# Performance work log

Measured on AMD Instinct MI355X. Metric: run time of the kernel, lower is better.

## Reference

```python
import jax, jax.numpy as jnp
import numpy as np
from jax import lax

NG = 2   # n_groups
NH = 4   # n_heads
LN_EPS = 1e-5

SOBEL_X = np.array([[-1., 0., 1.], [-2., 0., 2.], [-1., 0., 1.]], np.float32)
SOBEL_Y = np.array([[-1., -2., -1.], [0., 0., 0.], [1., 2., 1.]], np.float32)


def conv1x1(x, w, b=None):
    # x: (N, Ci, H, W), w: (Co, Ci)
    y = jnp.einsum('oi,bihw->bohw', w, x)
    if b is not None:
        y = y + b[None, :, None, None]
    return y


def dwconv3(x, w, b=None):
    # depthwise 3x3, stride 1, padding 1. w: (C, 1, 3, 3)
    y = lax.conv_general_dilated(x, w, (1, 1), ((1, 1), (1, 1)),
                                 feature_group_count=x.shape[1],
                                 dimension_numbers=('NCHW', 'OIHW', 'NCHW'))
    if b is not None:
        y = y + b[None, :, None, None]
    return y


def grid_sample_bilinear(img, grid):
    # img: (N, C, H, W); grid: (N, Hg, Wg, 2) with (x, y) in [-1, 1]
    # align_corners=True, zero padding (matches F.grid_sample defaults used here)
    N, C, H, W = img.shape
    gx = (grid[..., 0] + 1.0) * 0.5 * (W - 1)
    gy = (grid[..., 1] + 1.0) * 0.5 * (H - 1)
    x0 = jnp.floor(gx)
    y0 = jnp.floor(gy)
    wx1 = gx - x0
    wy1 = gy - y0

    def gather(yy, xx):
        valid = (yy >= 0) & (yy < H) & (xx >= 0) & (xx < W)
        yc = jnp.clip(yy, 0, H - 1).astype(jnp.int32)
        xc = jnp.clip(xx, 0, W - 1).astype(jnp.int32)
        vals = jax.vmap(lambda im, y_, x_: im[:, y_, x_])(img, yc, xc)  # (N,C,Hg,Wg)
        return vals * valid[:, None, :, :].astype(img.dtype)

    v00 = gather(y0, x0)
    v01 = gather(y0, x0 + 1)
    v10 = gather(y0 + 1, x0)
    v11 = gather(y0 + 1, x0 + 1)
    w00 = ((1 - wy1) * (1 - wx1))[:, None]
    w01 = ((1 - wy1) * wx1)[:, None]
    w10 = (wy1 * (1 - wx1))[:, None]
    w11 = (wy1 * wx1)[:, None]
    return v00 * w00 + v01 * w01 + v10 * w10 + v11 * w11


def setup_inputs() -> dict:
    key = jax.random.key(0)
    B, C, H, W = 4, 128, 48, 48
    Cg = C // NG
    ks = jax.random.split(key, 16)
    s = 0.02
    inp = {
        'x': jax.random.normal(ks[0], (B, C, H, W), jnp.float32),
        'qW': jax.random.normal(ks[1], (C, C), jnp.float32) * s,
        'qb': jnp.zeros((C,), jnp.float32),
        'kW': jax.random.normal(ks[2], (C, C), jnp.float32) * s,
        'kb': jnp.zeros((C,), jnp.float32),
        'vW': jax.random.normal(ks[3], (C, C), jnp.float32) * s,
        'vb': jnp.zeros((C,), jnp.float32),
        'oW': jax.random.normal(ks[4], (C, C), jnp.float32) * s,
        'ob': jnp.zeros((C,), jnp.float32),
        'off_dw_w': jax.random.normal(ks[5], (Cg, 1, 3, 3), jnp.float32) * 0.1,
        'off_dw_b': jnp.zeros((Cg,), jnp.float32),
        'ln_g': jnp.ones((Cg,), jnp.float32),
        'ln_b': jnp.zeros((Cg,), jnp.float32),
        'off_pw_w': jax.random.normal(ks[6], (2, Cg), jnp.float32) * s,
        'sob_w': jax.random.normal(ks[7], (1, Cg), jnp.float32) * 0.1,
        'sob_b': jnp.zeros((1,), jnp.float32),
        'rpe_w': jax.random.normal(ks[8], (C, 1, 3, 3), jnp.float32) * 0.1,
        'rpe_b': jnp.zeros((C,), jnp.float32),
    }
    return inp


def reference(x, qW, qb, kW, kb, vW, vb, oW, ob, off_dw_w, off_dw_b,
              ln_g, ln_b, off_pw_w, sob_w, sob_b, rpe_w, rpe_b):
    B, C, H, W = x.shape
    Cg = C // NG
    Dh = C // NH
    scale = Dh ** -0.5

    q = conv1x1(x, qW, qb)                                   # (B,C,H,W)
    q_off = q.reshape(B * NG, Cg, H, W)                      # (Bg,Cg,H,W)

    # offset branch: dwconv -> LayerNorm(channel) -> GELU -> 1x1 (no bias)
    t = dwconv3(q_off, off_dw_w, off_dw_b)
    tt = t.transpose(0, 2, 3, 1)                             # (Bg,H,W,Cg)
    mu = tt.mean(-1, keepdims=True)
    var = tt.var(-1, keepdims=True)
    tt = (tt - mu) / jnp.sqrt(var + LN_EPS) * ln_g + ln_b
    t = jax.nn.gelu(tt, approximate=False).transpose(0, 3, 1, 2)
    offset = conv1x1(t, off_pw_w)                            # (Bg,2,H,W)

    Hk, Wk = H, W
    n_sample = Hk * Wk
    off_range = jnp.array([1.0 / (Hk - 1.0), 1.0 / (Wk - 1.0)], x.dtype).reshape(1, 2, 1, 1)
    offset = jnp.tanh(offset) * off_range                    # offset_range_factor = 1
    offset = offset.transpose(0, 2, 3, 1)                    # (Bg,Hk,Wk,2)  (y,x)

    # reference points, normalized to [-1,1]
    ref_y = (jnp.linspace(0.5, Hk - 0.5, Hk, dtype=x.dtype) / (Hk - 1.0)) * 2.0 - 1.0
    ref_x = (jnp.linspace(0.5, Wk - 0.5, Wk, dtype=x.dtype) / (Wk - 1.0)) * 2.0 - 1.0
    ref = jnp.stack(jnp.meshgrid(ref_y, ref_x, indexing='ij'), axis=-1)  # (Hk,Wk,2)
    reference = jnp.broadcast_to(ref[None], (B * NG, Hk, Wk, 2))

    # Sobel gate on 1x1-projected q_off
    s = conv1x1(q_off, sob_w, sob_b)                         # (Bg,1,H,W)
    kx = jnp.asarray(SOBEL_X).reshape(1, 1, 3, 3)
    ky = jnp.asarray(SOBEL_Y).reshape(1, 1, 3, 3)
    gxm = dwconv3(s, kx)
    gym = dwconv3(s, ky)
    mag = jnp.sqrt(gxm ** 2 + gym ** 2)
    binary = (mag > 0.5).astype(x.dtype).transpose(0, 2, 3, 1)  # (Bg,H,W,1)

    pos = offset + reference * binary                        # (Bg,Hk,Wk,2) (y,x)

    xs = grid_sample_bilinear(x.reshape(B * NG, Cg, H, W), pos[..., ::-1])  # grid in (x,y)
    xs = xs.reshape(B, C, 1, n_sample)

    qf = q.reshape(B * NH, Dh, H * W)
    k = conv1x1(xs, kW, kb).reshape(B * NH, Dh, n_sample)
    v = conv1x1(xs, vW, vb).reshape(B * NH, Dh, n_sample)

    attn = jnp.einsum('bcm,bcn->bmn', qf, k) * scale         # (B*NH, HW, n_sample)
    lepe = dwconv3(q.reshape(B, C, H, W), rpe_w, rpe_b).reshape(B * NH, Dh, H * W)
    attn = jax.nn.softmax(attn, axis=2)                      # attn_drop: eval identity
    out = jnp.einsum('bmn,bcn->bcm', attn, v) + lepe
    out = out.reshape(B, C, H, W)
    y = conv1x1(out, oW, ob)                                 # proj_drop: eval identity
    return (y, pos, reference)
```

## Files before the change

### kernel.cpp

```cpp
#include <hip/hip_runtime.h>
#include <hip/hip_bf16.h>
#include <math.h>

#define B_   4
#define C_   128
#define H_   48
#define W_   48
#define HW_  2304
#define CG_  64
#define DH_  32
#define SCALE_ 0.17677669529663687f
#define QS_    (0.17677669529663687f * 1.4426950408889634f)
#define INVQ_  (1.0f / QS_)

#define Y_OFF   0
#define POS_OFF 1179648
#define REF_OFF 1216512

#define OFF_XTBF  0
#define OFF_QBF   589824
#define OFF_KBF   1179648
#define OFF_VBF   1769472
#define OFF_XST   2359296
#define OFF_WBF   2949120
#define OFF_PRS   2981888
#define OFF_PROH  4161536
#define OFF_AOUTT 6594560
#define OFF_SMAPD 7184384
#define OFF_WEFF  7221248

typedef __attribute__((ext_vector_type(8))) short short8;
typedef __attribute__((ext_vector_type(4))) float f32x4;
typedef __attribute__((ext_vector_type(4))) _Float16 f16x4;

__device__ inline unsigned short f2bf(float f) {
  unsigned u = __float_as_uint(f);
  u += 0x7fff + ((u >> 16) & 1);
  return (unsigned short)(u >> 16);
}
__device__ inline float bf2f(unsigned short s) {
  return __uint_as_float(((unsigned)s) << 16);
}

__device__ inline short8 pack8(const f32x4 a, const f32x4 b) {
  union { unsigned u[4]; short8 s; } r;
  asm("v_cvt_pk_bf16_f32 %0, %1, %2" : "=v"(r.u[0]) : "v"(a[0]), "v"(a[1]));
  asm("v_cvt_pk_bf16_f32 %0, %1, %2" : "=v"(r.u[1]) : "v"(a[2]), "v"(a[3]));
  asm("v_cvt_pk_bf16_f32 %0, %1, %2" : "=v"(r.u[2]) : "v"(b[0]), "v"(b[1]));
  asm("v_cvt_pk_bf16_f32 %0, %1, %2" : "=v"(r.u[3]) : "v"(b[2]), "v"(b[3]));
  return r.s;
}

__global__ __launch_bounds__(256) void k_pre(const float* __restrict__ x,
                                             const float* __restrict__ qW, const float* __restrict__ kW,
                                             const float* __restrict__ vW, const float* __restrict__ oW,
                                             const float* __restrict__ qb,
                                             const float* __restrict__ sob_w, const float* __restrict__ sob_b,
                                             unsigned short* __restrict__ xTbf,
                                             unsigned short* __restrict__ wbf,
                                             double* __restrict__ weff) {
  int bx = blockIdx.x;
  if (bx < 288) {
    __shared__ float tile[64][65];
    int p0 = (bx % 36) * 64, c0 = ((bx / 36) & 1) * 64, b = bx / 72;
    for (int idx = threadIdx.x; idx < 4096; idx += 256) {
      int cr = idx >> 6, pc = idx & 63;
      tile[cr][pc] = x[((size_t)(b * C_) + c0 + cr) * HW_ + p0 + pc];
    }
    __syncthreads();
    for (int idx = threadIdx.x; idx < 4096; idx += 256) {
      int pr = idx >> 6, cc = idx & 63;
      xTbf[((size_t)(b * HW_) + p0 + pr) * C_ + c0 + cc] = f2bf(tile[cc][pr]);
    }
  } else if (bx < 544) {
    int t = (bx - 288) * 256 + threadIdx.x;
    int which = t >> 14, i = t & 16383;
    const float* src = which == 0 ? qW : which == 1 ? kW : which == 2 ? vW : oW;
    wbf[t] = f2bf(src[i]);
  } else {
    int t = threadIdx.x;
    int g = t >> 7, i = t & 127;
    double acc = 0.0;
    for (int c = 0; c < 64; c++)
      acc += (double)sob_w[c] * (double)qW[(size_t)(g * 64 + c) * C_ + i];
    weff[t] = acc;
    if (t < 2) {
      double bb = (double)sob_b[0];
      for (int c = 0; c < 64; c++) bb += (double)sob_w[c] * (double)qb[t * 64 + c];
      weff[256 + t] = bb;
    }
  }
}

__global__ __launch_bounds__(256, 4) void k_qconv_smapd(const unsigned short* __restrict__ xTbf,
                                                        const unsigned short* __restrict__ wbf,
                                                        const float* __restrict__ qb,
                                                        const float* __restrict__ x,
                                                        const double* __restrict__ weff,
                                                        unsigned short* __restrict__ qbf,
                                                        double* __restrict__ smapd) {
  int bx = blockIdx.x;
  if (bx < 576) {
    int t = threadIdx.x, w = t >> 6, l = t & 63, lg = l >> 4, lo = l & 15;
    int m0 = (bx % 144) * 16, b = bx / 144, o0 = w * 32;
    const unsigned short* xrow = xTbf + ((size_t)(b * HW_) + m0 + lo) * C_ + lg * 8;
    f32x4 acc[2] = {{0.f,0.f,0.f,0.f},{0.f,0.f,0.f,0.f}};
#pragma unroll
    for (int kb = 0; kb < 4; kb++) {
      short8 xf = *(const short8*)(xrow + kb * 32);
#pragma unroll
      for (int os = 0; os < 2; os++) {
        short8 wf = *(const short8*)(wbf + (size_t)(o0 + os * 16 + lo) * C_ + kb * 32 + lg * 8);
        acc[os] = __builtin_amdgcn_mfma_f32_16x16x32_bf16(xf, wf, acc[os], 0, 0, 0);
      }
    }
#pragma unroll
    for (int os = 0; os < 2; os++) {
      int o = o0 + os * 16 + lo;
      float bi = qb[o];
#pragma unroll
      for (int r = 0; r < 4; r++) {
        int m = m0 + lg * 4 + r;
        qbf[((size_t)(b * HW_) + m) * C_ + o] = f2bf((acc[os][r] + bi) * QS_);
      }
    }
  } else {
    int bb = bx - 576;
    int p = (bb % 9) * 256 + threadIdx.x;
    int bg = bb / 9;
    int b = bg >> 1, g = bg & 1;
    const float* xb = x + (size_t)b * C_ * HW_ + p;
    const double* wv = weff + g * 128;
    double acc = weff[256 + g];
#pragma unroll 8
    for (int i = 0; i < 128; i++) acc += wv[i] * (double)xb[(size_t)i * HW_];
    smapd[bg * HW_ + p] = acc;
  }
}

__global__ __launch_bounds__(256) void k_offpos_sample(const unsigned short* __restrict__ qbf,
                                                       const double* __restrict__ s_map,
                                                       const float* __restrict__ dw_w,
                                                       const float* __restrict__ dw_b,
                                                       const float* __restrict__ ln_g,
                                                       const float* __restrict__ ln_b,
                                                       const float* __restrict__ pw_w,
                                                       const unsigned short* __restrict__ xTbf,
                                                       float* __restrict__ out,
                                                       unsigned short* __restrict__ xsT) {
  int widx = blockIdx.x * 4 + (threadIdx.x >> 6);
  int lane = threadIdx.x & 63;
  int bg = widx / HW_;
  int p = widx - bg * HW_;
  int h = p / W_, w = p - h * W_;
  int b = bg >> 1, g = bg & 1;
  const unsigned short* qc = qbf + (size_t)(b * HW_) * C_ + g * 64 + lane;
  float tv = dw_b[lane];
#pragma unroll
  for (int dy = -1; dy <= 1; dy++)
#pragma unroll
    for (int dx = -1; dx <= 1; dx++) {
      int hh = h + dy, ww = w + dx;
      if (hh >= 0 && hh < H_ && ww >= 0 && ww < W_) {
        float wgt = dw_w[lane * 9 + (dy + 1) * 3 + (dx + 1)] * INVQ_;
        tv += wgt * bf2f(qc[(size_t)(hh * W_ + ww) * C_]);
      }
    }
  float ssum = tv, ssq = tv * tv;
#pragma unroll
  for (int msk = 32; msk; msk >>= 1) {
    ssum += __shfl_xor(ssum, msk, 64);
    ssq  += __shfl_xor(ssq,  msk, 64);
  }
  float mu  = ssum * (1.0f / 64.0f);
  float var = ssq * (1.0f / 64.0f) - mu * mu;
  float uu  = (tv - mu) * rsqrtf(var + 1e-5f) * ln_g[lane] + ln_b[lane];
  float gl = 0.5f * uu * (1.0f + erff(uu * 0.70710678118654752f));
  float p0 = pw_w[lane] * gl, p1 = pw_w[64 + lane] * gl;
#pragma unroll
  for (int msk = 32; msk; msk >>= 1) {
    p0 += __shfl_xor(p0, msk, 64);
    p1 += __shfl_xor(p1, msk, 64);
  }
  const double sobx[9] = {-1., 0., 1., -2., 0., 2., -1., 0., 1.};
  const double soby[9] = {-1., -2., -1., 0., 0., 0., 1., 2., 1.};
  float off_y = tanhf(p0) * (1.0f / 47.0f);
  float off_x = tanhf(p1) * (1.0f / 47.0f);
  const double* sm = s_map + bg * HW_;
  double gx = 0., gy = 0.;
#pragma unroll
  for (int dy = -1; dy <= 1; dy++)
#pragma unroll
    for (int dx = -1; dx <= 1; dx++) {
      int hh = h + dy, ww = w + dx;
      if (hh >= 0 && hh < H_ && ww >= 0 && ww < W_) {
        double sv = sm[hh * W_ + ww];
        gx += sobx[(dy + 1) * 3 + dx + 1] * sv;
        gy += soby[(dy + 1) * 3 + dx + 1] * sv;
      }
    }
  double mag = sqrt(gx * gx + gy * gy);
  float bin = mag > 0.5 ? 1.0f : 0.0f;
  float ry = ((h + 0.5f) / 47.0f) * 2.0f - 1.0f;
  float rx = ((w + 0.5f) / 47.0f) * 2.0f - 1.0f;
  float py = off_y + ry * bin;
  float px = off_x + rx * bin;
  if (lane == 0) {
    int pi = (bg * HW_ + p) * 2;
    out[POS_OFF + pi]     = py;
    out[POS_OFF + pi + 1] = px;
    out[REF_OFF + pi]     = ry;
    out[REF_OFF + pi + 1] = rx;
  }
  float gxf = (px + 1.0f) * 0.5f * 47.0f;
  float gyf = (py + 1.0f) * 0.5f * 47.0f;
  float x0 = floorf(gxf), y0 = floorf(gyf);
  float wx1 = gxf - x0, wy1 = gyf - y0;
  float wx0 = 1.0f - wx1, wy0 = 1.0f - wy1;
  const unsigned short* base = xTbf + (size_t)(b * HW_) * C_ + g * 64 + lane;
  float acc = 0.0f;
#pragma unroll
  for (int cy = 0; cy < 2; cy++)
#pragma unroll
    for (int cx = 0; cx < 2; cx++) {
      float yy = y0 + (float)cy, xx = x0 + (float)cx;
      bool valid = (yy >= 0.f) && (yy < 48.f) && (xx >= 0.f) && (xx < 48.f);
      int yc = min(max((int)yy, 0), 47);
      int xc = min(max((int)xx, 0), 47);
      float wgt = (cy ? wy1 : wy0) * (cx ? wx1 : wx0);
      float vv = valid ? bf2f(base[(size_t)(yc * 48 + xc) * C_]) : 0.0f;
      acc += wgt * vv;
    }
  xsT[((size_t)(b * HW_) + p) * C_ + g * 64 + lane] = f2bf(acc);
}

__global__ __launch_bounds__(256, 4) void k_kvconv(const unsigned short* __restrict__ xsT,
                                                   const unsigned short* __restrict__ wbf,
                                                   const float* __restrict__ kbias,
                                                   const float* __restrict__ vbias,
                                                   unsigned short* __restrict__ kbf,
                                                   unsigned short* __restrict__ vbf) {
  int t = threadIdx.x, w = t >> 6, l = t & 63, lg = l >> 4, lo = l & 15;
  int n0 = blockIdx.x * 16, b = blockIdx.y, o0 = w * 32;
  const unsigned short* xrow = xsT + ((size_t)(b * HW_) + n0 + lo) * C_ + lg * 8;
  const unsigned short* wk = wbf + 16384;
  const unsigned short* wv = wbf + 32768;
  f32x4 ak[2] = {{0.f,0.f,0.f,0.f},{0.f,0.f,0.f,0.f}};
  f32x4 av[2] = {{0.f,0.f,0.f,0.f},{0.f,0.f,0.f,0.f}};
#pragma unroll
  for (int kb = 0; kb < 4; kb++) {
    short8 xf = *(const short8*)(xrow + kb * 32);
#pragma unroll
    for (int os = 0; os < 2; os++) {
      size_t wo = (size_t)(o0 + os * 16 + lo) * C_ + kb * 32 + lg * 8;
      short8 wkf = *(const short8*)(wk + wo);
      short8 wvf = *(const short8*)(wv + wo);
      ak[os] = __builtin_amdgcn_mfma_f32_16x16x32_bf16(xf, wkf, ak[os], 0, 0, 0);
      av[os] = __builtin_amdgcn_mfma_f32_16x16x32_bf16(wvf, xf, av[os], 0, 0, 0);
    }
  }
  int o32 = (n0 & 16) + lo;
  int vpos = (n0 & ~31) + ((o32 & 12) << 1) + (o32 & 3) + ((o32 >> 4) << 2);
#pragma unroll
  for (int os = 0; os < 2; os++) {
    int ok = o0 + os * 16 + lo;
    float bk_ = kbias[ok];
#pragma unroll
    for (int r = 0; r < 4; r++) {
      int n = n0 + lg * 4 + r;
      kbf[((size_t)(b * HW_) + n) * C_ + ok] = f2bf(ak[os][r] + bk_);
      int ov = o0 + os * 16 + lg * 4 + r;
      vbf[((size_t)(b * C_) + ov) * HW_ + vpos] = f2bf(av[os][r] + vbias[ov]);
    }
  }
}

#define EXPROW(SV, RS)                                                              \
  _Pragma("unroll")                                                                 \
  for (int r = 0; r < 4; r++) {                                                     \
    float e0, e1, e2, e3;                                                           \
    asm("v_exp_f32 %0, %1" : "=v"(e0) : "v"(SV##0[r]));                             \
    asm("v_exp_f32 %0, %1" : "=v"(e1) : "v"(SV##1[r]));                             \
    asm("v_exp_f32 %0, %1" : "=v"(e2) : "v"(SV##2[r]));                             \
    asm("v_exp_f32 %0, %1" : "=v"(e3) : "v"(SV##3[r]));                             \
    SV##0[r] = e0; SV##1[r] = e1; SV##2[r] = e2; SV##3[r] = e3;                     \
    RS += (e0 + e1) + (e2 + e3);                                                    \
  }

#define ATTN_BODY5(BK, BKN, DOPREF)                                                 \
  {                                                                                 \
    short8 bv0 = *(const short8*)(vr0 + n0);                                        \
    short8 bv1 = *(const short8*)(vr0 + n0 + 32);                                   \
    short8 bv2 = *(const short8*)(vr1 + n0);                                        \
    short8 bv3 = *(const short8*)(vr1 + n0 + 32);                                   \
    if (DOPREF) {                                                                   \
      _Pragma("unroll")                                                             \
      for (int sub = 0; sub < 4; sub++)                                             \
        BKN[sub] = *(const short8*)(kb_ + (size_t)(n0 + 64 + sub * 16 + lo) * C_);  \
    }                                                                               \
    f32x4 z = {0.f, 0.f, 0.f, 0.f};                                                 \
    __builtin_amdgcn_s_setprio(1);                                                  \
    f32x4 s0 = __builtin_amdgcn_mfma_f32_16x16x32_bf16(BK[0], aq0, z, 0, 0, 0);     \
    f32x4 s1 = __builtin_amdgcn_mfma_f32_16x16x32_bf16(BK[1], aq0, z, 0, 0, 0);     \
    f32x4 s2 = __builtin_amdgcn_mfma_f32_16x16x32_bf16(BK[2], aq0, z, 0, 0, 0);     \
    f32x4 s3 = __builtin_amdgcn_mfma_f32_16x16x32_bf16(BK[3], aq0, z, 0, 0, 0);     \
    __builtin_amdgcn_s_setprio(0);                                                  \
    EXPROW(s, rsum0)                                                                \
    short8 pa0 = pack8(s0, s1), pa1 = pack8(s2, s3);                                \
    __builtin_amdgcn_s_setprio(1);                                                  \
    f32x4 t0 = __builtin_amdgcn_mfma_f32_16x16x32_bf16(BK[0], aq1, z, 0, 0, 0);     \
    f32x4 t1 = __builtin_amdgcn_mfma_f32_16x16x32_bf16(BK[1], aq1, z, 0, 0, 0);     \
    f32x4 t2 = __builtin_amdgcn_mfma_f32_16x16x32_bf16(BK[2], aq1, z, 0, 0, 0);     \
    f32x4 t3 = __builtin_amdgcn_mfma_f32_16x16x32_bf16(BK[3], aq1, z, 0, 0, 0);     \
    acc00 = __builtin_amdgcn_mfma_f32_16x16x32_bf16(pa0, bv0, acc00, 0, 0, 0);      \
    acc00 = __builtin_amdgcn_mfma_f32_16x16x32_bf16(pa1, bv1, acc00, 0, 0, 0);      \
    acc01 = __builtin_amdgcn_mfma_f32_16x16x32_bf16(pa0, bv2, acc01, 0, 0, 0);      \
    acc01 = __builtin_amdgcn_mfma_f32_16x16x32_bf16(pa1, bv3, acc01, 0, 0, 0);      \
    __builtin_amdgcn_s_setprio(0);                                                  \
    EXPROW(t, rsum1)                                                                \
    short8 pb0 = pack8(t0, t1), pb1 = pack8(t2, t3);                                \
    __builtin_amdgcn_s_setprio(1);                                                  \
    acc10 = __builtin_amdgcn_mfma_f32_16x16x32_bf16(pb0, bv0, acc10, 0, 0, 0);      \
    acc10 = __builtin_amdgcn_mfma_f32_16x16x32_bf16(pb1, bv1, acc10, 0, 0, 0);      \
    acc11 = __builtin_amdgcn_mfma_f32_16x16x32_bf16(pb0, bv2, acc11, 0, 0, 0);      \
    acc11 = __builtin_amdgcn_mfma_f32_16x16x32_bf16(pb1, bv3, acc11, 0, 0, 0);      \
    __builtin_amdgcn_s_setprio(0);                                                  \
    n0 += 64;                                                                       \
  }

__global__ __launch_bounds__(256, 3) void k_attn5(const unsigned short* __restrict__ qbf,
                                                  const unsigned short* __restrict__ kbf,
                                                  const unsigned short* __restrict__ vpf,
                                                  _Float16* __restrict__ prOh,
                                                  float* __restrict__ prS) {
  int t = threadIdx.x, w = t >> 6, l = t & 63, lg = l >> 4, lo = l & 15;
  int bh = blockIdx.y, b = bh >> 2, hd = bh & 3, nz = blockIdx.z;
  int cb = hd * 32;
  int m0 = blockIdx.x * 128 + w * 32;
  const unsigned short* qrow = qbf + ((size_t)(b * HW_) + m0 + lo) * C_ + cb + lg * 8;
  short8 aq0 = *(const short8*)qrow;
  short8 aq1 = *(const short8*)(qrow + (size_t)16 * C_);
  const unsigned short* kb_ = kbf + (size_t)(b * HW_) * C_ + cb + lg * 8;
  const unsigned short* vr0 = vpf + (size_t)(b * C_ + cb + lo) * HW_ + lg * 8;
  const unsigned short* vr1 = vr0 + (size_t)16 * HW_;
  f32x4 acc00 = {0.f,0.f,0.f,0.f}, acc01 = {0.f,0.f,0.f,0.f};
  f32x4 acc10 = {0.f,0.f,0.f,0.f}, acc11 = {0.f,0.f,0.f,0.f};
  float rsum0 = 0.f, rsum1 = 0.f;
  int n0 = nz * 576;
  short8 bkA[4], bkB[4];
#pragma unroll
  for (int sub = 0; sub < 4; sub++)
    bkA[sub] = *(const short8*)(kb_ + (size_t)(n0 + sub * 16 + lo) * C_);
  for (int i4 = 0; i4 < 4; i4++) {
    ATTN_BODY5(bkA, bkB, true)
    ATTN_BODY5(bkB, bkA, (i4 < 3))
  }
  ATTN_BODY5(bkA, bkB, false)
  rsum0 += __shfl_xor(rsum0, 16, 64);
  rsum0 += __shfl_xor(rsum0, 32, 64);
  rsum1 += __shfl_xor(rsum1, 16, 64);
  rsum1 += __shfl_xor(rsum1, 32, 64);
  _Float16* pr = prOh + (size_t)nz * (B_ * HW_ * C_);
#pragma unroll
  for (int r = 0; r < 4; r++) {
    int m = m0 + lg * 4 + r;
    size_t oi = ((size_t)(b * HW_) + m) * C_ + cb;
    pr[oi + lo] = (_Float16)acc00[r];
    pr[oi + 16 + lo] = (_Float16)acc01[r];
    size_t oi2 = oi + (size_t)16 * C_;
    pr[oi2 + lo] = (_Float16)acc10[r];
    pr[oi2 + 16 + lo] = (_Float16)acc11[r];
  }
  if (l < 16) {
    prS[((size_t)(nz * 16) + bh) * HW_ + m0 + lo] = rsum0;
    prS[((size_t)(nz * 16) + bh) * HW_ + m0 + 16 + lo] = rsum1;
  }
}

__global__ __launch_bounds__(256) void k_combine2(const _Float16* __restrict__ prOh,
                                                  const float* __restrict__ prS,
                                                  const unsigned short* __restrict__ qbf,
                                                  const float* __restrict__ rpe_w,
                                                  const float* __restrict__ rpe_b,
                                                  unsigned short* __restrict__ aoutT) {
  size_t oi = ((size_t)blockIdx.x * 256 + threadIdx.x) * 4;
  int c = (int)(oi & 127);
  size_t bm = oi >> 7;
  int b = (int)(bm / HW_);
  int m = (int)(bm - (size_t)b * HW_);
  int hd = c >> 5;
  int bh = b * 4 + hd;
  float rs = 0.f;
  float o[4] = {0.f, 0.f, 0.f, 0.f};
#pragma unroll
  for (int nz = 0; nz < 4; nz++) {
    rs += prS[((size_t)(nz * 16) + bh) * HW_ + m];
    f16x4 v = *(const f16x4*)(prOh + (size_t)nz * (B_ * HW_ * C_) + oi);
#pragma unroll
    for (int j = 0; j < 4; j++) o[j] += (float)v[j];
  }
  float inv = 1.0f / rs;
  int h = m / W_, w = m - (m / W_) * W_;
  float lp[4] = {rpe_b[c], rpe_b[c + 1], rpe_b[c + 2], rpe_b[c + 3]};
#pragma unroll
  for (int dy = -1; dy <= 1; dy++)
#pragma unroll
    for (int dx = -1; dx <= 1; dx++) {
      int hh = h + dy, ww = w + dx;
      if (hh >= 0 && hh < H_ && ww >= 0 && ww < W_) {
        int idx = (dy + 1) * 3 + (dx + 1);
        ushort4 q4 = *(const ushort4*)(qbf + ((size_t)(b * HW_) + hh * W_ + ww) * C_ + c);
        lp[0] += rpe_w[(c + 0) * 9 + idx] * INVQ_ * bf2f(q4.x);
        lp[1] += rpe_w[(c + 1) * 9 + idx] * INVQ_ * bf2f(q4.y);
        lp[2] += rpe_w[(c + 2) * 9 + idx] * INVQ_ * bf2f(q4.z);
        lp[3] += rpe_w[(c + 3) * 9 + idx] * INVQ_ * bf2f(q4.w);
      }
    }
  ushort4 pk;
  pk.x = f2bf(o[0] * inv + lp[0]);
  pk.y = f2bf(o[1] * inv + lp[1]);
  pk.z = f2bf(o[2] * inv + lp[2]);
  pk.w = f2bf(o[3] * inv + lp[3]);
  *(ushort4*)(aoutT + oi) = pk;
}

__global__ __launch_bounds__(256, 4) void k_oconv(const unsigned short* __restrict__ aoutT,
                                                  const unsigned short* __restrict__ wbf,
                                                  const float* __restrict__ ob_,
                                                  float* __restrict__ y) {
  int t = threadIdx.x, w = t >> 6, l = t & 63, lg = l >> 4, lo = l & 15;
  int m0 = blockIdx.x * 16, b = blockIdx.y, o0 = w * 32;
  const unsigned short* xrow = aoutT + ((size_t)(b * HW_) + m0 + lo) * C_ + lg * 8;
  const unsigned short* wo = wbf + 49152;
  f32x4 acc[2] = {{0.f,0.f,0.f,0.f},{0.f,0.f,0.f,0.f}};
#pragma unroll
  for (int kb = 0; kb < 4; kb++) {
    short8 xf = *(const short8*)(xrow + kb * 32);
#pragma unroll
    for (int os = 0; os < 2; os++) {
      short8 wf = *(const short8*)(wo + (size_t)(o0 + os * 16 + lo) * C_ + kb * 32 + lg * 8);
      acc[os] = __builtin_amdgcn_mfma_f32_16x16x32_bf16(wf, xf, acc[os], 0, 0, 0);
    }
  }
#pragma unroll
  for (int os = 0; os < 2; os++)
#pragma unroll
    for (int r = 0; r < 4; r++) {
      int o = o0 + os * 16 + lg * 4 + r;
      y[((size_t)(b * C_) + o) * HW_ + m0 + lo] = acc[os][r] + ob_[o];
    }
}

extern "C" void kernel_launch(void* const* d_in, const int* in_sizes, int n_in,
                              void* d_out, int out_size, void* d_ws, size_t ws_size,
                              hipStream_t stream) {
  const float* x        = (const float*)d_in[0];
  const float* qW       = (const float*)d_in[1];
  const float* qb       = (const float*)d_in[2];
  const float* kW       = (const float*)d_in[3];
  const float* kb       = (const float*)d_in[4];
  const float* vW       = (const float*)d_in[5];
  const float* vb       = (const float*)d_in[6];
  const float* oW       = (const float*)d_in[7];
  const float* ob       = (const float*)d_in[8];
  const float* off_dw_w = (const float*)d_in[9];
  const float* off_dw_b = (const float*)d_in[10];
  const float* ln_g     = (const float*)d_in[11];
  const float* ln_b     = (const float*)d_in[12];
  const float* off_pw_w = (const float*)d_in[13];
  const float* sob_w    = (const float*)d_in[14];
  const float* sob_b    = (const float*)d_in[15];
  const float* rpe_w    = (const float*)d_in[16];
  const float* rpe_b    = (const float*)d_in[17];
  float* out = (float*)d_out;
  float* wsf = (float*)d_ws;
  unsigned short* xTbf  = (unsigned short*)(wsf + OFF_XTBF);
  unsigned short* qbf   = (unsigned short*)(wsf + OFF_QBF);
  unsigned short* kbf   = (unsigned short*)(wsf + OFF_KBF);
  unsigned short* vbf   = (unsigned short*)(wsf + OFF_VBF);
  unsigned short* xsT   = (unsigned short*)(wsf + OFF_XST);
  unsigned short* wbf   = (unsigned short*)(wsf + OFF_WBF);
  unsigned short* aoutT = (unsigned short*)(wsf + OFF_AOUTT);
  float* prS   = wsf + OFF_PRS;
  _Float16* prOh = (_Float16*)(wsf + OFF_PROH);
  double* smapd = (double*)(wsf + OFF_SMAPD);
  double* weff  = (double*)(wsf + OFF_WEFF);

  k_pre          <<<545,             256, 0, stream>>>(x, qW, kW, vW, oW, qb, sob_w, sob_b,
                                                       xTbf, wbf, weff);
  k_qconv_smapd  <<<648,             256, 0, stream>>>(xTbf, wbf, qb, x, weff, qbf, smapd);
  k_offpos_sample<<<4608,            256, 0, stream>>>(qbf, smapd, off_dw_w, off_dw_b,
                                                       ln_g, ln_b, off_pw_w, xTbf, out, xsT);
  k_kvconv       <<<dim3(144, 4),    256, 0, stream>>>(xsT, wbf, kb, vb, kbf, vbf);
  k_attn5        <<<dim3(18, 16, 4), 256, 0, stream>>>(qbf, kbf, vbf, prOh, prS);
  k_combine2     <<<1152,            256, 0, stream>>>(prOh, prS, qbf, rpe_w, rpe_b, aoutT);
  k_oconv        <<<dim3(144, 4),    256, 0, stream>>>(aoutT, wbf, ob, out + Y_OFF);
}
```

Measured before the change: 124.6 us.

## Give each attention wave 64 query rows and fuse combine with output projection

The attention kernel now assigns 64 query rows per wavefront instead of 32, using 128-thread blocks, so each K/V fragment load feeds four QK^T/PV tiles rather than two. This halves K/V load traffic per query. The separate combine and output-projection kernels are merged into one. The normalized attention-plus-LePE tile is staged in shared memory and fed straight into the MFMA projection, which removes the aoutT round trip and one launch. The cost is more accumulator registers per wave and fewer waves per block, which may reduce occupancy and latency hiding.

```diff
diff --git a/kernel.cpp b/kernel.cpp
--- a/kernel.cpp
+++ b/kernel.cpp
@@ -25,13 +25,13 @@
 #define OFF_WBF   2949120
 #define OFF_PRS   2981888
 #define OFF_PROH  4161536
-#define OFF_AOUTT 6594560
 #define OFF_SMAPD 7184384
 #define OFF_WEFF  7221248
 
 typedef __attribute__((ext_vector_type(8))) short short8;
 typedef __attribute__((ext_vector_type(4))) float f32x4;
 typedef __attribute__((ext_vector_type(4))) _Float16 f16x4;
+typedef __attribute__((ext_vector_type(8))) _Float16 f16x8;
 
 __device__ inline unsigned short f2bf(float f) {
   unsigned u = __float_as_uint(f);
@@ -275,19 +275,31 @@
   }
 }
 
-#define EXPROW(SV, RS)                                                              \
+#define EXPROW2(S0, S1, S2, S3, RS)                                                 \
   _Pragma("unroll")                                                                 \
   for (int r = 0; r < 4; r++) {                                                     \
     float e0, e1, e2, e3;                                                           \
-    asm("v_exp_f32 %0, %1" : "=v"(e0) : "v"(SV##0[r]));                             \
-    asm("v_exp_f32 %0, %1" : "=v"(e1) : "v"(SV##1[r]));                             \
-    asm("v_exp_f32 %0, %1" : "=v"(e2) : "v"(SV##2[r]));                             \
-    asm("v_exp_f32 %0, %1" : "=v"(e3) : "v"(SV##3[r]));                             \
-    SV##0[r] = e0; SV##1[r] = e1; SV##2[r] = e2; SV##3[r] = e3;                     \
+    asm("v_exp_f32 %0, %1" : "=v"(e0) : "v"(S0[r]));                                \
+    asm("v_exp_f32 %0, %1" : "=v"(e1) : "v"(S1[r]));                                \
+    asm("v_exp_f32 %0, %1" : "=v"(e2) : "v"(S2[r]));                                \
+    asm("v_exp_f32 %0, %1" : "=v"(e3) : "v"(S3[r]));                                \
+    S0[r] = e0; S1[r] = e1; S2[r] = e2; S3[r] = e3;                                 \
     RS += (e0 + e1) + (e2 + e3);                                                    \
   }
 
-#define ATTN_BODY5(BK, BKN, DOPREF)                                                 \
+#define QKT(BK, AQ, S0, S1, S2, S3)                                                 \
+    S0 = __builtin_amdgcn_mfma_f32_16x16x32_bf16(BK[0], AQ, z, 0, 0, 0);            \
+    S1 = __builtin_amdgcn_mfma_f32_16x16x32_bf16(BK[1], AQ, z, 0, 0, 0);            \
+    S2 = __builtin_amdgcn_mfma_f32_16x16x32_bf16(BK[2], AQ, z, 0, 0, 0);            \
+    S3 = __builtin_amdgcn_mfma_f32_16x16x32_bf16(BK[3], AQ, z, 0, 0, 0);
+
+#define PVT(PA0, PA1, AL, AH)                                                       \
+    AL = __builtin_amdgcn_mfma_f32_16x16x32_bf16(PA0, bv0, AL, 0, 0, 0);            \
+    AL = __builtin_amdgcn_mfma_f32_16x16x32_bf16(PA1, bv1, AL, 0, 0, 0);            \
+    AH = __builtin_amdgcn_mfma_f32_16x16x32_bf16(PA0, bv2, AH, 0, 0, 0);            \
+    AH = __builtin_amdgcn_mfma_f32_16x16x32_bf16(PA1, bv3, AH, 0, 0, 0);
+
+#define ATTN_BODY6(BK, BKN, DOPREF)                                                 \
   {                                                                                 \
     short8 bv0 = *(const short8*)(vr0 + n0);                                        \
     short8 bv1 = *(const short8*)(vr0 + n0 + 32);                                   \
@@ -299,36 +311,37 @@
         BKN[sub] = *(const short8*)(kb_ + (size_t)(n0 + 64 + sub * 16 + lo) * C_);  \
     }                                                                               \
     f32x4 z = {0.f, 0.f, 0.f, 0.f};                                                 \
+    f32x4 s0, s1, s2, s3, t0, t1, t2, t3;                                           \
     __builtin_amdgcn_s_setprio(1);                                                  \
-    f32x4 s0 = __builtin_amdgcn_mfma_f32_16x16x32_bf16(BK[0], aq0, z, 0, 0, 0);     \
-    f32x4 s1 = __builtin_amdgcn_mfma_f32_16x16x32_bf16(BK[1], aq0, z, 0, 0, 0);     \
-    f32x4 s2 = __builtin_amdgcn_mfma_f32_16x16x32_bf16(BK[2], aq0, z, 0, 0, 0);     \
-    f32x4 s3 = __builtin_amdgcn_mfma_f32_16x16x32_bf16(BK[3], aq0, z, 0, 0, 0);     \
+    QKT(BK, aq0, s0, s1, s2, s3)                                                    \
     __builtin_amdgcn_s_setprio(0);                                                  \
-    EXPROW(s, rsum0)                                                                \
+    EXPROW2(s0, s1, s2, s3, rsv[0])                                                 \
     short8 pa0 = pack8(s0, s1), pa1 = pack8(s2, s3);                                \
     __builtin_amdgcn_s_setprio(1);                                                  \
-    f32x4 t0 = __builtin_amdgcn_mfma_f32_16x16x32_bf16(BK[0], aq1, z, 0, 0, 0);     \
-    f32x4 t1 = __builtin_amdgcn_mfma_f32_16x16x32_bf16(BK[1], aq1, z, 0, 0, 0);     \
-    f32x4 t2 = __builtin_amdgcn_mfma_f32_16x16x32_bf16(BK[2], aq1, z, 0, 0, 0);     \
-    f32x4 t3 = __builtin_amdgcn_mfma_f32_16x16x32_bf16(BK[3], aq1, z, 0, 0, 0);     \
-    acc00 = __builtin_amdgcn_mfma_f32_16x16x32_bf16(pa0, bv0, acc00, 0, 0, 0);      \
-    acc00 = __builtin_amdgcn_mfma_f32_16x16x32_bf16(pa1, bv1, acc00, 0, 0, 0);      \
-    acc01 = __builtin_amdgcn_mfma_f32_16x16x32_bf16(pa0, bv2, acc01, 0, 0, 0);      \
-    acc01 = __builtin_amdgcn_mfma_f32_16x16x32_bf16(pa1, bv3, acc01, 0, 0, 0);      \
+    QKT(BK, aq1, t0, t1, t2, t3)                                                    \
+    PVT(pa0, pa1, aL[0], aH[0])                                                     \
     __builtin_amdgcn_s_setprio(0);                                                  \
-    EXPROW(t, rsum1)                                                                \
+    EXPROW2(t0, t1, t2, t3, rsv[1])                                                 \
     short8 pb0 = pack8(t0, t1), pb1 = pack8(t2, t3);                                \
     __builtin_amdgcn_s_setprio(1);                                                  \
-    acc10 = __builtin_amdgcn_mfma_f32_16x16x32_bf16(pb0, bv0, acc10, 0, 0, 0);      \
-    acc10 = __builtin_amdgcn_mfma_f32_16x16x32_bf16(pb1, bv1, acc10, 0, 0, 0);      \
-    acc11 = __builtin_amdgcn_mfma_f32_16x16x32_bf16(pb0, bv2, acc11, 0, 0, 0);      \
-    acc11 = __builtin_amdgcn_mfma_f32_16x16x32_bf16(pb1, bv3, acc11, 0, 0, 0);      \
+    QKT(BK, aq2, s0, s1, s2, s3)                                                    \
+    PVT(pb0, pb1, aL[1], aH[1])                                                     \
+    __builtin_amdgcn_s_setprio(0);                                                  \
+    EXPROW2(s0, s1, s2, s3, rsv[2])                                                 \
+    short8 pc0 = pack8(s0, s1), pc1 = pack8(s2, s3);                                \
+    __builtin_amdgcn_s_setprio(1);                                                  \
+    QKT(BK, aq3, t0, t1, t2, t3)                                                    \
+    PVT(pc0, pc1, aL[2], aH[2])                                                     \
+    __builtin_amdgcn_s_setprio(0);                                                  \
+    EXPROW2(t0, t1, t2, t3, rsv[3])                                                 \
+    short8 pd0 = pack8(t0, t1), pd1 = pack8(t2, t3);                                \
+    __builtin_amdgcn_s_setprio(1);                                                  \
+    PVT(pd0, pd1, aL[3], aH[3])                                                     \
     __builtin_amdgcn_s_setprio(0);                                                  \
     n0 += 64;                                                                       \
   }
 
-__global__ __launch_bounds__(256, 3) void k_attn5(const unsigned short* __restrict__ qbf,
+__global__ __launch_bounds__(128, 2) void k_attn6(const unsigned short* __restrict__ qbf,
                                                   const unsigned short* __restrict__ kbf,
                                                   const unsigned short* __restrict__ vpf,
                                                   _Float16* __restrict__ prOh,
@@ -336,106 +349,107 @@
   int t = threadIdx.x, w = t >> 6, l = t & 63, lg = l >> 4, lo = l & 15;
   int bh = blockIdx.y, b = bh >> 2, hd = bh & 3, nz = blockIdx.z;
   int cb = hd * 32;
-  int m0 = blockIdx.x * 128 + w * 32;
+  int m0 = blockIdx.x * 128 + w * 64;
   const unsigned short* qrow = qbf + ((size_t)(b * HW_) + m0 + lo) * C_ + cb + lg * 8;
   short8 aq0 = *(const short8*)qrow;
   short8 aq1 = *(const short8*)(qrow + (size_t)16 * C_);
+  short8 aq2 = *(const short8*)(qrow + (size_t)32 * C_);
+  short8 aq3 = *(const short8*)(qrow + (size_t)48 * C_);
   const unsigned short* kb_ = kbf + (size_t)(b * HW_) * C_ + cb + lg * 8;
   const unsigned short* vr0 = vpf + (size_t)(b * C_ + cb + lo) * HW_ + lg * 8;
   const unsigned short* vr1 = vr0 + (size_t)16 * HW_;
-  f32x4 acc00 = {0.f,0.f,0.f,0.f}, acc01 = {0.f,0.f,0.f,0.f};
-  f32x4 acc10 = {0.f,0.f,0.f,0.f}, acc11 = {0.f,0.f,0.f,0.f};
-  float rsum0 = 0.f, rsum1 = 0.f;
+  f32x4 aL[4] = {{0.f,0.f,0.f,0.f},{0.f,0.f,0.f,0.f},{0.f,0.f,0.f,0.f},{0.f,0.f,0.f,0.f}};
+  f32x4 aH[4] = {{0.f,0.f,0.f,0.f},{0.f,0.f,0.f,0.f},{0.f,0.f,0.f,0.f},{0.f,0.f,0.f,0.f}};
+  f32x4 rsv = {0.f, 0.f, 0.f, 0.f};
   int n0 = nz * 576;
   short8 bkA[4], bkB[4];
 #pragma unroll
   for (int sub = 0; sub < 4; sub++)
     bkA[sub] = *(const short8*)(kb_ + (size_t)(n0 + sub * 16 + lo) * C_);
   for (int i4 = 0; i4 < 4; i4++) {
-    ATTN_BODY5(bkA, bkB, true)
-    ATTN_BODY5(bkB, bkA, (i4 < 3))
-  }
-  ATTN_BODY5(bkA, bkB, false)
-  rsum0 += __shfl_xor(rsum0, 16, 64);
-  rsum0 += __shfl_xor(rsum0, 32, 64);
-  rsum1 += __shfl_xor(rsum1, 16, 64);
-  rsum1 += __shfl_xor(rsum1, 32, 64);
+    ATTN_BODY6(bkA, bkB, true)
+    ATTN_BODY6(bkB, bkA, (i4 < 3))
+  }
+  ATTN_BODY6(bkA, bkB, false)
+#pragma unroll
+  for (int qi = 0; qi < 4; qi++) {
+    rsv[qi] += __shfl_xor(rsv[qi], 16, 64);
+    rsv[qi] += __shfl_xor(rsv[qi], 32, 64);
+  }
   _Float16* pr = prOh + (size_t)nz * (B_ * HW_ * C_);
 #pragma unroll
-  for (int r = 0; r < 4; r++) {
-    int m = m0 + lg * 4 + r;
-    size_t oi = ((size_t)(b * HW_) + m) * C_ + cb;
-    pr[oi + lo] = (_Float16)acc00[r];
-    pr[oi + 16 + lo] = (_Float16)acc01[r];
-    size_t oi2 = oi + (size_t)16 * C_;
-    pr[oi2 + lo] = (_Float16)acc10[r];
-    pr[oi2 + 16 + lo] = (_Float16)acc11[r];
+  for (int qi = 0; qi < 4; qi++) {
+#pragma unroll
+    for (int r = 0; r < 4; r++) {
+      int m = m0 + qi * 16 + lg * 4 + r;
+      size_t oi = ((size_t)(b * HW_) + m) * C_ + cb;
+      pr[oi + lo] = (_Float16)aL[qi][r];
+      pr[oi + 16 + lo] = (_Float16)aH[qi][r];
+    }
   }
   if (l < 16) {
-    prS[((size_t)(nz * 16) + bh) * HW_ + m0 + lo] = rsum0;
-    prS[((size_t)(nz * 16) + bh) * HW_ + m0 + 16 + lo] = rsum1;
-  }
-}
-
-__global__ __launch_bounds__(256) void k_combine2(const _Float16* __restrict__ prOh,
-                                                  const float* __restrict__ prS,
-                                                  const unsigned short* __restrict__ qbf,
-                                                  const float* __restrict__ rpe_w,
-                                                  const float* __restrict__ rpe_b,
-                                                  unsigned short* __restrict__ aoutT) {
-  size_t oi = ((size_t)blockIdx.x * 256 + threadIdx.x) * 4;
-  int c = (int)(oi & 127);
-  size_t bm = oi >> 7;
-  int b = (int)(bm / HW_);
-  int m = (int)(bm - (size_t)b * HW_);
-  int hd = c >> 5;
-  int bh = b * 4 + hd;
-  float rs = 0.f;
-  float o[4] = {0.f, 0.f, 0.f, 0.f};
-#pragma unroll
-  for (int nz = 0; nz < 4; nz++) {
-    rs += prS[((size_t)(nz * 16) + bh) * HW_ + m];
-    f16x4 v = *(const f16x4*)(prOh + (size_t)nz * (B_ * HW_ * C_) + oi);
-#pragma unroll
-    for (int j = 0; j < 4; j++) o[j] += (float)v[j];
-  }
-  float inv = 1.0f / rs;
-  int h = m / W_, w = m - (m / W_) * W_;
-  float lp[4] = {rpe_b[c], rpe_b[c + 1], rpe_b[c + 2], rpe_b[c + 3]};
-#pragma unroll
-  for (int dy = -1; dy <= 1; dy++)
-#pragma unroll
-    for (int dx = -1; dx <= 1; dx++) {
-      int hh = h + dy, ww = w + dx;
-      if (hh >= 0 && hh < H_ && ww >= 0 && ww < W_) {
-        int idx = (dy + 1) * 3 + (dx + 1);
-        ushort4 q4 = *(const ushort4*)(qbf + ((size_t)(b * HW_) + hh * W_ + ww) * C_ + c);
-        lp[0] += rpe_w[(c + 0) * 9 + idx] * INVQ_ * bf2f(q4.x);
-        lp[1] += rpe_w[(c + 1) * 9 + idx] * INVQ_ * bf2f(q4.y);
-        lp[2] += rpe_w[(c + 2) * 9 + idx] * INVQ_ * bf2f(q4.z);
-        lp[3] += rpe_w[(c + 3) * 9 + idx] * INVQ_ * bf2f(q4.w);
+#pragma unroll
+    for (int qi = 0; qi < 4; qi++)
+      prS[((size_t)(nz * 16) + bh) * HW_ + m0 + qi * 16 + lo] = rsv[qi];
+  }
+}
+
+__global__ __launch_bounds__(256) void k_out(const _Float16* __restrict__ prOh,
+                                             const float* __restrict__ prS,
+                                             const unsigned short* __restrict__ qbf,
+                                             const float* __restrict__ rpe_w,
+                                             const float* __restrict__ rpe_b,
+                                             const unsigned short* __restrict__ wbf,
+                                             const float* __restrict__ ob_,
+                                             float* __restrict__ y) {
+  __shared__ __align__(16) unsigned short lds[16][136];
+  int t = threadIdx.x;
+  int m0 = blockIdx.x * 16, b = blockIdx.y;
+  {
+    int mi = t >> 4, c8 = (t & 15) * 8;
+    int m = m0 + mi;
+    int hd = c8 >> 5;
+    size_t oi = ((size_t)(b * HW_) + m) * C_ + c8;
+    float rs = 0.f;
+    float o[8] = {0.f,0.f,0.f,0.f,0.f,0.f,0.f,0.f};
+#pragma unroll
+    for (int nz = 0; nz < 4; nz++) {
+      rs += prS[((size_t)(nz * 16) + b * 4 + hd) * HW_ + m];
+      f16x8 v = *(const f16x8*)(prOh + (size_t)nz * (B_ * HW_ * C_) + oi);
+#pragma unroll
+      for (int j = 0; j < 8; j++) o[j] += (float)v[j];
+    }
+    float inv = 1.0f / rs;
+    int h = m / W_, ww0 = m - h * W_;
+    float lp[8];
+#pragma unroll
+    for (int j = 0; j < 8; j++) lp[j] = rpe_b[c8 + j];
+#pragma unroll
+    for (int dy = -1; dy <= 1; dy++)
+#pragma unroll
+      for (int dx = -1; dx <= 1; dx++) {
+        int hh = h + dy, ww = ww0 + dx;
+        if (hh >= 0 && hh < H_ && ww >= 0 && ww < W_) {
+          int idx = (dy + 1) * 3 + (dx + 1);
+          short8 q8 = *(const short8*)(qbf + ((size_t)(b * HW_) + hh * W_ + ww) * C_ + c8);
+#pragma unroll
+          for (int j = 0; j < 8; j++)
+            lp[j] += rpe_w[(c8 + j) * 9 + idx] * INVQ_ * bf2f((unsigned short)q8[j]);
+        }
       }
-    }
-  ushort4 pk;
-  pk.x = f2bf(o[0] * inv + lp[0]);
-  pk.y = f2bf(o[1] * inv + lp[1]);
-  pk.z = f2bf(o[2] * inv + lp[2]);
-  pk.w = f2bf(o[3] * inv + lp[3]);
-  *(ushort4*)(aoutT + oi) = pk;
-}
-
-__global__ __launch_bounds__(256, 4) void k_oconv(const unsigned short* __restrict__ aoutT,
-                                                  const unsigned short* __restrict__ wbf,
-                                                  const float* __restrict__ ob_,
-                                                  float* __restrict__ y) {
-  int t = threadIdx.x, w = t >> 6, l = t & 63, lg = l >> 4, lo = l & 15;
-  int m0 = blockIdx.x * 16, b = blockIdx.y, o0 = w * 32;
-  const unsigned short* xrow = aoutT + ((size_t)(b * HW_) + m0 + lo) * C_ + lg * 8;
+    short8 res;
+#pragma unroll
+    for (int j = 0; j < 8; j++) res[j] = (short)f2bf(o[j] * inv + lp[j]);
+    *(short8*)&lds[mi][c8] = res;
+  }
+  __syncthreads();
+  int w = t >> 6, l = t & 63, lg = l >> 4, lo = l & 15;
+  int o0 = w * 32;
   const unsigned short* wo = wbf + 49152;
   f32x4 acc[2] = {{0.f,0.f,0.f,0.f},{0.f,0.f,0.f,0.f}};
 #pragma unroll
   for (int kb = 0; kb < 4; kb++) {
-    short8 xf = *(const short8*)(xrow + kb * 32);
+    short8 xf = *(const short8*)&lds[lo][kb * 32 + lg * 8];
 #pragma unroll
     for (int os = 0; os < 2; os++) {
       short8 wf = *(const short8*)(wo + (size_t)(o0 + os * 16 + lo) * C_ + kb * 32 + lg * 8);
@@ -480,7 +494,6 @@
   unsigned short* vbf   = (unsigned short*)(wsf + OFF_VBF);
   unsigned short* xsT   = (unsigned short*)(wsf + OFF_XST);
   unsigned short* wbf   = (unsigned short*)(wsf + OFF_WBF);
-  unsigned short* aoutT = (unsigned short*)(wsf + OFF_AOUTT);
   float* prS   = wsf + OFF_PRS;
   _Float16* prOh = (_Float16*)(wsf + OFF_PROH);
   double* smapd = (double*)(wsf + OFF_SMAPD);
@@ -492,7 +505,7 @@
   k_offpos_sample<<<4608,            256, 0, stream>>>(qbf, smapd, off_dw_w, off_dw_b,
                                                        ln_g, ln_b, off_pw_w, xTbf, out, xsT);
   k_kvconv       <<<dim3(144, 4),    256, 0, stream>>>(xsT, wbf, kb, vb, kbf, vbf);
-  k_attn5        <<<dim3(18, 16, 4), 256, 0, stream>>>(qbf, kbf, vbf, prOh, prS);
-  k_combine2     <<<1152,            256, 0, stream>>>(prOh, prS, qbf, rpe_w, rpe_b, aoutT);
-  k_oconv        <<<dim3(144, 4),    256, 0, stream>>>(aoutT, wbf, ob, out + Y_OFF);
-}
+  k_attn6        <<<dim3(18, 16, 4), 128, 0, stream>>>(qbf, kbf, vbf, prOh, prS);
+  k_out          <<<dim3(144, 4),    256, 0, stream>>>(prOh, prS, qbf, rpe_w, rpe_b,
+                                                       wbf, ob, out + Y_OFF);
+}
```

Result: faster. 119.8 us (-3.9%).

## Fuse split-K combine with output projection, split attention six ways, prefetch V

Applied to the files above, without the earlier changes.

The split-K attention now divides the key range into six chunks instead of four, giving more blocks for occupancy. V fragments are double-buffered and prefetched along with K. The combine kernel (partial sum reduction plus LePE depthwise conv) is fused into the output 1x1 conv through LDS, which removes the aoutT intermediate round-trip and one launch. The cost is more partial buffers to read and reduce in the combine step.

```diff
diff --git a/kernel.cpp b/kernel.cpp
--- a/kernel.cpp
+++ b/kernel.cpp
@@ -9,6 +9,7 @@
 #define HW_  2304
 #define CG_  64
 #define DH_  32
+#define NZ_  6
 #define SCALE_ 0.17677669529663687f
 #define QS_    (0.17677669529663687f * 1.4426950408889634f)
 #define INVQ_  (1.0f / QS_)
@@ -24,14 +25,14 @@
 #define OFF_XST   2359296
 #define OFF_WBF   2949120
 #define OFF_PRS   2981888
-#define OFF_PROH  4161536
-#define OFF_AOUTT 6594560
-#define OFF_SMAPD 7184384
-#define OFF_WEFF  7221248
+#define OFF_PROH  3203072
+#define OFF_SMAPD 6742016
+#define OFF_WEFF  6778880
 
 typedef __attribute__((ext_vector_type(8))) short short8;
 typedef __attribute__((ext_vector_type(4))) float f32x4;
 typedef __attribute__((ext_vector_type(4))) _Float16 f16x4;
+typedef __attribute__((ext_vector_type(8))) _Float16 f16x8;
 
 __device__ inline unsigned short f2bf(float f) {
   unsigned u = __float_as_uint(f);
@@ -287,16 +288,16 @@
     RS += (e0 + e1) + (e2 + e3);                                                    \
   }
 
-#define ATTN_BODY5(BK, BKN, DOPREF)                                                 \
+#define ATTN_BODY7(BK, BV, BKN, BVN, DOPREF)                                        \
   {                                                                                 \
-    short8 bv0 = *(const short8*)(vr0 + n0);                                        \
-    short8 bv1 = *(const short8*)(vr0 + n0 + 32);                                   \
-    short8 bv2 = *(const short8*)(vr1 + n0);                                        \
-    short8 bv3 = *(const short8*)(vr1 + n0 + 32);                                   \
     if (DOPREF) {                                                                   \
       _Pragma("unroll")                                                             \
       for (int sub = 0; sub < 4; sub++)                                             \
         BKN[sub] = *(const short8*)(kb_ + (size_t)(n0 + 64 + sub * 16 + lo) * C_);  \
+      BVN[0] = *(const short8*)(vr0 + n0 + 64);                                     \
+      BVN[1] = *(const short8*)(vr0 + n0 + 96);                                     \
+      BVN[2] = *(const short8*)(vr1 + n0 + 64);                                     \
+      BVN[3] = *(const short8*)(vr1 + n0 + 96);                                     \
     }                                                                               \
     f32x4 z = {0.f, 0.f, 0.f, 0.f};                                                 \
     __builtin_amdgcn_s_setprio(1);                                                  \
@@ -312,23 +313,23 @@
     f32x4 t1 = __builtin_amdgcn_mfma_f32_16x16x32_bf16(BK[1], aq1, z, 0, 0, 0);     \
     f32x4 t2 = __builtin_amdgcn_mfma_f32_16x16x32_bf16(BK[2], aq1, z, 0, 0, 0);     \
     f32x4 t3 = __builtin_amdgcn_mfma_f32_16x16x32_bf16(BK[3], aq1, z, 0, 0, 0);     \
-    acc00 = __builtin_amdgcn_mfma_f32_16x16x32_bf16(pa0, bv0, acc00, 0, 0, 0);      \
-    acc00 = __builtin_amdgcn_mfma_f32_16x16x32_bf16(pa1, bv1, acc00, 0, 0, 0);      \
-    acc01 = __builtin_amdgcn_mfma_f32_16x16x32_bf16(pa0, bv2, acc01, 0, 0, 0);      \
-    acc01 = __builtin_amdgcn_mfma_f32_16x16x32_bf16(pa1, bv3, acc01, 0, 0, 0);      \
+    acc00 = __builtin_amdgcn_mfma_f32_16x16x32_bf16(pa0, BV[0], acc00, 0, 0, 0);    \
+    acc00 = __builtin_amdgcn_mfma_f32_16x16x32_bf16(pa1, BV[1], acc00, 0, 0, 0);    \
+    acc01 = __builtin_amdgcn_mfma_f32_16x16x32_bf16(pa0, BV[2], acc01, 0, 0, 0);    \
+    acc01 = __builtin_amdgcn_mfma_f32_16x16x32_bf16(pa1, BV[3], acc01, 0, 0, 0);    \
     __builtin_amdgcn_s_setprio(0);                                                  \
     EXPROW(t, rsum1)                                                                \
     short8 pb0 = pack8(t0, t1), pb1 = pack8(t2, t3);                                \
     __builtin_amdgcn_s_setprio(1);                                                  \
-    acc10 = __builtin_amdgcn_mfma_f32_16x16x32_bf16(pb0, bv0, acc10, 0, 0, 0);      \
-    acc10 = __builtin_amdgcn_mfma_f32_16x16x32_bf16(pb1, bv1, acc10, 0, 0, 0);      \
-    acc11 = __builtin_amdgcn_mfma_f32_16x16x32_bf16(pb0, bv2, acc11, 0, 0, 0);      \
-    acc11 = __builtin_amdgcn_mfma_f32_16x16x32_bf16(pb1, bv3, acc11, 0, 0, 0);      \
+    acc10 = __builtin_amdgcn_mfma_f32_16x16x32_bf16(pb0, BV[0], acc10, 0, 0, 0);    \
+    acc10 = __builtin_amdgcn_mfma_f32_16x16x32_bf16(pb1, BV[1], acc10, 0, 0, 0);    \
+    acc11 = __builtin_amdgcn_mfma_f32_16x16x32_bf16(pb0, BV[2], acc11, 0, 0, 0);    \
+    acc11 = __builtin_amdgcn_mfma_f32_16x16x32_bf16(pb1, BV[3], acc11, 0, 0, 0);    \
     __builtin_amdgcn_s_setprio(0);                                                  \
     n0 += 64;                                                                       \
   }
 
-__global__ __launch_bounds__(256, 3) void k_attn5(const unsigned short* __restrict__ qbf,
+__global__ __launch_bounds__(256, 3) void k_attn7(const unsigned short* __restrict__ qbf,
                                                   const unsigned short* __restrict__ kbf,
                                                   const unsigned short* __restrict__ vpf,
                                                   _Float16* __restrict__ prOh,
@@ -346,16 +347,19 @@
   f32x4 acc00 = {0.f,0.f,0.f,0.f}, acc01 = {0.f,0.f,0.f,0.f};
   f32x4 acc10 = {0.f,0.f,0.f,0.f}, acc11 = {0.f,0.f,0.f,0.f};
   float rsum0 = 0.f, rsum1 = 0.f;
-  int n0 = nz * 576;
-  short8 bkA[4], bkB[4];
+  int n0 = nz * 384;
+  short8 bkA[4], bkB[4], bvA[4], bvB[4];
 #pragma unroll
   for (int sub = 0; sub < 4; sub++)
     bkA[sub] = *(const short8*)(kb_ + (size_t)(n0 + sub * 16 + lo) * C_);
-  for (int i4 = 0; i4 < 4; i4++) {
-    ATTN_BODY5(bkA, bkB, true)
-    ATTN_BODY5(bkB, bkA, (i4 < 3))
-  }
-  ATTN_BODY5(bkA, bkB, false)
+  bvA[0] = *(const short8*)(vr0 + n0);
+  bvA[1] = *(const short8*)(vr0 + n0 + 32);
+  bvA[2] = *(const short8*)(vr1 + n0);
+  bvA[3] = *(const short8*)(vr1 + n0 + 32);
+  for (int i3 = 0; i3 < 3; i3++) {
+    ATTN_BODY7(bkA, bvA, bkB, bvB, true)
+    ATTN_BODY7(bkB, bvB, bkA, bvA, (i3 < 2))
+  }
   rsum0 += __shfl_xor(rsum0, 16, 64);
   rsum0 += __shfl_xor(rsum0, 32, 64);
   rsum1 += __shfl_xor(rsum1, 16, 64);
@@ -377,65 +381,62 @@
   }
 }
 
-__global__ __launch_bounds__(256) void k_combine2(const _Float16* __restrict__ prOh,
-                                                  const float* __restrict__ prS,
-                                                  const unsigned short* __restrict__ qbf,
-                                                  const float* __restrict__ rpe_w,
-                                                  const float* __restrict__ rpe_b,
-                                                  unsigned short* __restrict__ aoutT) {
-  size_t oi = ((size_t)blockIdx.x * 256 + threadIdx.x) * 4;
-  int c = (int)(oi & 127);
-  size_t bm = oi >> 7;
-  int b = (int)(bm / HW_);
-  int m = (int)(bm - (size_t)b * HW_);
-  int hd = c >> 5;
-  int bh = b * 4 + hd;
-  float rs = 0.f;
-  float o[4] = {0.f, 0.f, 0.f, 0.f};
-#pragma unroll
-  for (int nz = 0; nz < 4; nz++) {
-    rs += prS[((size_t)(nz * 16) + bh) * HW_ + m];
-    f16x4 v = *(const f16x4*)(prOh + (size_t)nz * (B_ * HW_ * C_) + oi);
-#pragma unroll
-    for (int j = 0; j < 4; j++) o[j] += (float)v[j];
-  }
-  float inv = 1.0f / rs;
-  int h = m / W_, w = m - (m / W_) * W_;
-  float lp[4] = {rpe_b[c], rpe_b[c + 1], rpe_b[c + 2], rpe_b[c + 3]};
-#pragma unroll
-  for (int dy = -1; dy <= 1; dy++)
-#pragma unroll
-    for (int dx = -1; dx <= 1; dx++) {
-      int hh = h + dy, ww = w + dx;
-      if (hh >= 0 && hh < H_ && ww >= 0 && ww < W_) {
-        int idx = (dy + 1) * 3 + (dx + 1);
-        ushort4 q4 = *(const ushort4*)(qbf + ((size_t)(b * HW_) + hh * W_ + ww) * C_ + c);
-        lp[0] += rpe_w[(c + 0) * 9 + idx] * INVQ_ * bf2f(q4.x);
-        lp[1] += rpe_w[(c + 1) * 9 + idx] * INVQ_ * bf2f(q4.y);
-        lp[2] += rpe_w[(c + 2) * 9 + idx] * INVQ_ * bf2f(q4.z);
-        lp[3] += rpe_w[(c + 3) * 9 + idx] * INVQ_ * bf2f(q4.w);
+__global__ __launch_bounds__(256) void k_out(const _Float16* __restrict__ prOh,
+                                             const float* __restrict__ prS,
+                                             const unsigned short* __restrict__ qbf,
+                                             const float* __restrict__ rpe_w,
+                                             const float* __restrict__ rpe_b,
+                                             const unsigned short* __restrict__ wbf,
+                                             const float* __restrict__ ob_,
+                                             float* __restrict__ y) {
+  __shared__ __align__(16) unsigned short lds[16][136];
+  int t = threadIdx.x;
+  int m0 = blockIdx.x * 16, b = blockIdx.y;
+  {
+    int mi = t >> 4, c8 = (t & 15) * 8;
+    int m = m0 + mi;
+    int hd = c8 >> 5;
+    size_t oi = ((size_t)(b * HW_) + m) * C_ + c8;
+    float rs = 0.f;
+    float o[8] = {0.f,0.f,0.f,0.f,0.f,0.f,0.f,0.f};
+#pragma unroll
+    for (int nz = 0; nz < NZ_; nz++) {
+      rs += prS[((size_t)(nz * 16) + b * 4 + hd) * HW_ + m];
+      f16x8 v = *(const f16x8*)(prOh + (size_t)nz * (B_ * HW_ * C_) + oi);
+#pragma unroll
+      for (int j = 0; j < 8; j++) o[j] += (float)v[j];
+    }
+    float inv = 1.0f / rs;
+    int h = m / W_, ww0 = m - h * W_;
+    float lp[8];
+#pragma unroll
+    for (int j = 0; j < 8; j++) lp[j] = rpe_b[c8 + j];
+#pragma unroll
+    for (int dy = -1; dy <= 1; dy++)
+#pragma unroll
+      for (int dx = -1; dx <= 1; dx++) {
+        int hh = h + dy, ww = ww0 + dx;
+        if (hh >= 0 && hh < H_ && ww >= 0 && ww < W_) {
+          int idx = (dy + 1) * 3 + (dx + 1);
+          short8 q8 = *(const short8*)(qbf + ((size_t)(b * HW_) + hh * W_ + ww) * C_ + c8);
+#pragma unroll
+          for (int j = 0; j < 8; j++)
+            lp[j] += rpe_w[(c8 + j) * 9 + idx] * INVQ_ * bf2f((unsigned short)q8[j]);
+        }
       }
-    }
-  ushort4 pk;
-  pk.x = f2bf(o[0] * inv + lp[0]);
-  pk.y = f2bf(o[1] * inv + lp[1]);
-  pk.z = f2bf(o[2] * inv + lp[2]);
-  pk.w = f2bf(o[3] * inv + lp[3]);
-  *(ushort4*)(aoutT + oi) = pk;
-}
-
-__global__ __launch_bounds__(256, 4) void k_oconv(const unsigned short* __restrict__ aoutT,
-                                                  const unsigned short* __restrict__ wbf,
-                                                  const float* __restrict__ ob_,
-                                                  float* __restrict__ y) {
-  int t = threadIdx.x, w = t >> 6, l = t & 63, lg = l >> 4, lo = l & 15;
-  int m0 = blockIdx.x * 16, b = blockIdx.y, o0 = w * 32;
-  const unsigned short* xrow = aoutT + ((size_t)(b * HW_) + m0 + lo) * C_ + lg * 8;
+    short8 res;
+#pragma unroll
+    for (int j = 0; j < 8; j++) res[j] = (short)f2bf(o[j] * inv + lp[j]);
+    *(short8*)&lds[mi][c8] = res;
+  }
+  __syncthreads();
+  int w = t >> 6, l = t & 63, lg = l >> 4, lo = l & 15;
+  int o0 = w * 32;
   const unsigned short* wo = wbf + 49152;
   f32x4 acc[2] = {{0.f,0.f,0.f,0.f},{0.f,0.f,0.f,0.f}};
 #pragma unroll
   for (int kb = 0; kb < 4; kb++) {
-    short8 xf = *(const short8*)(xrow + kb * 32);
+    short8 xf = *(const short8*)&lds[lo][kb * 32 + lg * 8];
 #pragma unroll
     for (int os = 0; os < 2; os++) {
       short8 wf = *(const short8*)(wo + (size_t)(o0 + os * 16 + lo) * C_ + kb * 32 + lg * 8);
@@ -480,7 +481,6 @@
   unsigned short* vbf   = (unsigned short*)(wsf + OFF_VBF);
   unsigned short* xsT   = (unsigned short*)(wsf + OFF_XST);
   unsigned short* wbf   = (unsigned short*)(wsf + OFF_WBF);
-  unsigned short* aoutT = (unsigned short*)(wsf + OFF_AOUTT);
   float* prS   = wsf + OFF_PRS;
   _Float16* prOh = (_Float16*)(wsf + OFF_PROH);
   double* smapd = (double*)(wsf + OFF_SMAPD);
@@ -492,7 +492,7 @@
   k_offpos_sample<<<4608,            256, 0, stream>>>(qbf, smapd, off_dw_w, off_dw_b,
                                                        ln_g, ln_b, off_pw_w, xTbf, out, xsT);
   k_kvconv       <<<dim3(144, 4),    256, 0, stream>>>(xsT, wbf, kb, vb, kbf, vbf);
-  k_attn5        <<<dim3(18, 16, 4), 256, 0, stream>>>(qbf, kbf, vbf, prOh, prS);
-  k_combine2     <<<1152,            256, 0, stream>>>(prOh, prS, qbf, rpe_w, rpe_b, aoutT);
-  k_oconv        <<<dim3(144, 4),    256, 0, stream>>>(aoutT, wbf, ob, out + Y_OFF);
-}
+  k_attn7        <<<dim3(18, 16, 6), 256, 0, stream>>>(qbf, kbf, vbf, prOh, prS);
+  k_out          <<<dim3(144, 4),    256, 0, stream>>>(prOh, prS, qbf, rpe_w, rpe_b,
+                                                       wbf, ob, out + Y_OFF);
+}
```

Measured after the change: 134.7 us. 8.1% more time.
